# Kernel optimization log

Measured on AMD Instinct MI355X. Metric: run time of the kernel, lower is better.

Reference implementation:

```python
import jax, jax.numpy as jnp
import numpy as np
from jax import lax
from jax.scipy.special import logsumexp

B, T, Lc = 64, 512, 16
DW, CD, NF, KS, H, K, CV = 300, 50, 100, 3, 256, 9, 100
SCALE = 0.05


def setup_inputs() -> dict:
    key = jax.random.key(0)
    ks = jax.random.split(key, 20)
    f32 = jnp.float32
    return {
        'word_embs': jax.random.normal(ks[0], (B, T, DW), f32),
        'chars': jax.random.randint(ks[1], (B, T, Lc), 0, CV),
        'lengths': jax.random.randint(ks[2], (B,), T // 2, T + 1).astype(jnp.int32),
        'tags': jax.random.randint(ks[3], (B, T), 0, K),
        'fin_W': jax.random.normal(ks[4], (DW, DW), f32) * SCALE,
        'fin_b': jnp.zeros((DW,), f32),
        'char_emb': jax.random.normal(ks[5], (CV, CD), f32) * SCALE,
        'conv_W': jax.random.normal(ks[6], (KS, CD, NF), f32) * SCALE,  # (W, In, Out)
        'conv_b': jnp.zeros((NF,), f32),
        'Wih_f': jax.random.normal(ks[7], (4 * H, DW + NF), f32) * SCALE,
        'Whh_f': jax.random.normal(ks[8], (4 * H, H), f32) * SCALE,
        'b_f': jnp.zeros((4 * H,), f32),
        'Wih_b': jax.random.normal(ks[9], (4 * H, DW + NF), f32) * SCALE,
        'Whh_b': jax.random.normal(ks[10], (4 * H, H), f32) * SCALE,
        'b_b': jnp.zeros((4 * H,), f32),
        'out_W': jax.random.normal(ks[11], (2 * H, K), f32) * SCALE,
        'out_b': jnp.zeros((K,), f32),
        'trans': jax.random.normal(ks[12], (K, K), f32) * SCALE,
        'start_trans': jax.random.normal(ks[13], (K,), f32) * SCALE,
        'end_trans': jax.random.normal(ks[14], (K,), f32) * SCALE,
    }


def _lstm_scan(x, mask, Wih, Whh, b):
    # x: [B,T,D], mask: [B,T] bool -> outputs [B,T,H] (zeros at padding)
    xT = jnp.swapaxes(x, 0, 1)              # [T,B,D]
    mT = jnp.swapaxes(mask, 0, 1)           # [T,B]
    pre = jnp.einsum('tbd,gd->tbg', xT, Wih) + b  # precompute input part [T,B,4H]
    h0 = jnp.zeros((x.shape[0], Whh.shape[1]), x.dtype)

    def step(carry, inp):
        h, c = carry
        px, m = inp
        g = px + h @ Whh.T
        i, f, gg, o = jnp.split(g, 4, axis=-1)  # pytorch gate order i,f,g,o
        c_new = jax.nn.sigmoid(f) * c + jax.nn.sigmoid(i) * jnp.tanh(gg)
        h_new = jax.nn.sigmoid(o) * jnp.tanh(c_new)
        m = m[:, None]
        h2 = jnp.where(m, h_new, h)
        c2 = jnp.where(m, c_new, c)
        return (h2, c2), h2 * m

    _, hs = lax.scan(step, (h0, h0), (pre, mT))
    return jnp.swapaxes(hs, 0, 1)


def _reverse_by_length(x, lengths):
    # reverse the valid prefix of each sequence (padding stays at the end)
    t = jnp.arange(x.shape[1])
    rev = jnp.where(t[None, :] < lengths[:, None], lengths[:, None] - 1 - t[None, :], t[None, :])
    return jnp.take_along_axis(x, rev[:, :, None], axis=1)


def _crf_forward(logits, tags, mask, trans, start_trans, end_trans):
    # torchcrf-style log-likelihood; returns scalar sum over batch
    eT = jnp.swapaxes(logits, 0, 1)  # [T,B,K]
    mT = jnp.swapaxes(mask, 0, 1).astype(logits.dtype)  # [T,B]
    bidx = jnp.arange(logits.shape[0])
    # numerator: gold path score
    score = start_trans[tags[:, 0]] + eT[0][bidx, tags[:, 0]]

    def nstep(carry, inp):
        sc, prev = carry
        e, tg, m = inp
        step_sc = trans[prev, tg] + e[bidx, tg]
        sc = sc + m * step_sc
        prev = jnp.where(m > 0, tg, prev)
        return (sc, prev), None

    tT = jnp.swapaxes(tags, 0, 1)
    (score, last_tag), _ = lax.scan(nstep, (score, tags[:, 0]), (eT[1:], tT[1:], mT[1:]))
    score = score + end_trans[last_tag]
    # denominator: log-partition via forward algorithm
    alpha = start_trans[None, :] + eT[0]

    def fstep(a, inp):
        e, m = inp
        nxt = logsumexp(a[:, :, None] + trans[None, :, :] + e[:, None, :], axis=1)
        return jnp.where(m[:, None] > 0, nxt, a), None

    alpha, _ = lax.scan(fstep, alpha, (eT[1:], mT[1:]))
    Z = logsumexp(alpha + end_trans[None, :], axis=-1)
    return jnp.sum(score - Z)


def _viterbi(logits, mask, trans, start_trans, end_trans):
    eT = jnp.swapaxes(logits, 0, 1)  # [T,B,K]
    mT = jnp.swapaxes(mask, 0, 1)    # [T,B] bool
    Ktags = logits.shape[-1]
    ident = jnp.arange(Ktags)[None, :]

    def vstep(a, inp):
        e, m = inp
        cand = a[:, :, None] + trans[None, :, :]   # [B, K_prev, K_cur]
        bp = jnp.argmax(cand, axis=1)
        nxt = jnp.max(cand, axis=1) + e
        a2 = jnp.where(m[:, None], nxt, a)
        bp = jnp.where(m[:, None], bp, ident)       # identity backptr at padding
        return a2, bp

    alpha, bps = lax.scan(vstep, start_trans[None, :] + eT[0], (eT[1:], mT[1:]))
    last = jnp.argmax(alpha + end_trans[None, :], axis=-1)

    def bstep(tag, bp):
        prev = jnp.take_along_axis(bp, tag[:, None], axis=1)[:, 0]
        return prev, tag

    tag0, tail = lax.scan(bstep, last, bps, reverse=True)  # tail[t] = tag at time t+1
    path = jnp.concatenate([tag0[:, None], jnp.swapaxes(tail, 0, 1)], axis=1)  # [B,T]
    return path * mask  # zero-pad like zero_pad(preds)


def reference(word_embs, chars, lengths, tags, fin_W, fin_b, char_emb, conv_W, conv_b,
              Wih_f, Whh_f, b_f, Wih_b, Whh_b, b_b, out_W, out_b,
              trans, start_trans, end_trans):
    mask = jnp.arange(T)[None, :] < lengths[:, None]  # [B,T]
    # 1) word embeddings through finetune linear
    we = word_embs @ fin_W.T + fin_b
    # 2) char CNN: embed -> conv1d over chars -> relu -> max-pool
    ce = char_emb[chars].reshape(B * T, Lc, CD)
    conv = lax.conv_general_dilated(ce, conv_W, (1,), 'SAME',
                                    dimension_numbers=('NWC', 'WIO', 'NWC')) + conv_b
    char_feat = jnp.max(jax.nn.relu(conv), axis=1).reshape(B, T, NF)
    # 3) concat; 4) BiLSTM (dropout=0 / eval mode)
    x = jnp.concatenate([we, char_feat], axis=-1)
    h_fwd = _lstm_scan(x, mask, Wih_f, Whh_f, b_f)
    x_rev = _reverse_by_length(x, lengths)
    h_bwd = _reverse_by_length(_lstm_scan(x_rev, mask, Wih_b, Whh_b, b_b), lengths)
    lstm_out = jnp.concatenate([h_fwd, h_bwd], axis=-1)  # [B,T,2H]
    # 5) linear head; 6-7) CRF loss + viterbi decode
    logits = lstm_out @ out_W + out_b  # [B,T,K]
    loss = -_crf_forward(logits, tags, mask, trans, start_trans, end_trans)
    preds = _viterbi(logits, mask, trans, start_trans, end_trans)
    return loss, preds
```

## Files before the change

kernel.cpp:

```cpp
#include <hip/hip_runtime.h>


__device__ __forceinline__ float sigf(float x){ return 1.0f/(1.0f + expf(-x)); }

__global__ void pack_weights(const float* __restrict__ Wih_f, const float* __restrict__ Wih_b,
                             const float* __restrict__ Whh_f, const float* __restrict__ Whh_b,
                             const float* __restrict__ fin_W,
                             float4* __restrict__ Wp_f, float4* __restrict__ Wp_b,
                             float4* __restrict__ WT_f, float4* __restrict__ WT_b,
                             float* __restrict__ finWT){
  int stride = gridDim.x*blockDim.x;
  for (int idx = blockIdx.x*blockDim.x + threadIdx.x; idx < 425872; idx += stride){
    if (idx < 204800){
      int i2 = idx; const float* W = Wih_f; float4* P = Wp_f;
      if (i2 >= 102400){ i2 -= 102400; W = Wih_b; P = Wp_b; }
      int d = i2 >> 8, j = i2 & 255;
      P[i2] = make_float4(W[j*400+d], W[(j+256)*400+d], W[(j+512)*400+d], W[(j+768)*400+d]);
    } else if (idx < 335872){
      int i2 = idx - 204800; const float* W = Whh_f; float4* P = WT_f;
      if (i2 >= 65536){ i2 -= 65536; W = Whh_b; P = WT_b; }
      int d = i2 >> 8, j = i2 & 255;
      P[i2] = make_float4(W[j*256+d], W[(j+256)*256+d], W[(j+512)*256+d], W[(j+768)*256+d]);
    } else {
      int i2 = idx - 335872;
      int d = i2 / 300, j = i2 - d*300;
      finWT[d*304 + j] = fin_W[j*300 + d];
    }
  }
}

__global__ __launch_bounds__(256) void featurize(const float* __restrict__ we_in,
      const float* __restrict__ finWT, const float* __restrict__ finb,
      const int* __restrict__ chars, const float* __restrict__ char_emb,
      const float* __restrict__ convW, const float* __restrict__ convb,
      float* __restrict__ x){
  __shared__ __align__(16) char fsm[31104];
  int bid = blockIdx.x;
  int tid = threadIdx.x;
  if (bid < 2048){
    float* embT = (float*)fsm;
    int tok0 = bid * 16;
    for (int idx = tid; idx < 4800; idx += 256){
      int tt = idx / 300, d = idx - tt*300;
      embT[d*16 + tt] = we_in[(size_t)tok0*300 + idx];
    }
    __syncthreads();
    for (int j = tid; j < 300; j += 256){
      float bias = finb[j];
      float acc[16];
#pragma unroll
      for (int k2=0;k2<16;k2++) acc[k2]=bias;
      const float4* e4 = (const float4*)embT;
#pragma unroll 4
      for (int d=0; d<300; d++){
        float w = finWT[d*304 + j];
        float4 a = e4[d*4+0], b2 = e4[d*4+1], c2 = e4[d*4+2], d2 = e4[d*4+3];
        acc[0]+=a.x*w;  acc[1]+=a.y*w;  acc[2]+=a.z*w;  acc[3]+=a.w*w;
        acc[4]+=b2.x*w; acc[5]+=b2.y*w; acc[6]+=b2.z*w; acc[7]+=b2.w*w;
        acc[8]+=c2.x*w; acc[9]+=c2.y*w; acc[10]+=c2.z*w;acc[11]+=c2.w*w;
        acc[12]+=d2.x*w;acc[13]+=d2.y*w;acc[14]+=d2.z*w;acc[15]+=d2.w*w;
      }
#pragma unroll
      for (int k2=0;k2<16;k2++) x[(size_t)(tok0+k2)*400 + j] = acc[k2];
    }
  } else {
    float* ce2 = (float*)fsm;
    int* chs = (int*)(fsm + 30464);
    int tok0 = (bid - 2048) * 8;
    if (tid < 128) chs[tid] = chars[(size_t)tok0*16 + tid];
    __syncthreads();
    for (int idx = tid; idx < 7200; idx += 256){
      int tok = idx / 900; int r = idx - tok*900;
      int w1 = r / 50; int c = r - w1*50;
      float v = 0.f;
      if (w1 >= 1 && w1 <= 16) v = char_emb[chs[tok*16 + (w1-1)]*50 + c];
      ce2[tok*952 + c*19 + w1] = v;
    }
    __syncthreads();
    for (int p = tid; p < 800; p += 256){
      int tok = p / 100, f = p - tok*100;
      float s[16];
#pragma unroll
      for (int w=0; w<16; w++) s[w] = 0.f;
      const float* cebase = ce2 + tok*952;
      for (int c=0; c<50; c++){
        float cr[18];
#pragma unroll
        for (int i=0;i<18;i++) cr[i] = cebase[c*19+i];
#pragma unroll
        for (int k2=0;k2<3;k2++){
          float wv = convW[(k2*50+c)*100 + f];
#pragma unroll
          for (int w=0;w<16;w++) s[w] += cr[w+k2]*wv;
        }
      }
      float m = s[0];
#pragma unroll
      for (int w=1;w<16;w++) m = fmaxf(m, s[w]);
      m = fmaxf(0.f, m + convb[f]);
      x[(size_t)(tok0+tok)*400 + 300 + f] = m;
    }
  }
}

__global__ __launch_bounds__(256) void pre_gemm(const float* __restrict__ x,
     const float4* __restrict__ Wp_f, const float4* __restrict__ Wp_b,
     const float* __restrict__ b_f, const float* __restrict__ b_b,
     const int* __restrict__ lengths,
     float4* __restrict__ pre_f, float4* __restrict__ pre_b,
     int t0, int CH){
  int dir = blockIdx.z;
  const float4* Wp = dir ? Wp_b : Wp_f;
  const float* bias = dir ? b_b : b_f;
  float4* pre = dir ? pre_b : pre_f;
  int tok0 = blockIdx.x * 64;
  int j0 = blockIdx.y * 64;
  __shared__ float As[16][68];
  __shared__ float4 Bs[4][16][16];
  __shared__ int rows_s[64];
  __shared__ int poss_s[64];
  int tid = threadIdx.x;
  int tx = tid & 15, ty = tid >> 4;
  if (tid < 64){
    int tok = tok0 + tid;
    int b = tok / CH;
    int trel = tok - b*CH;
    int t = t0 + trel;
    int row;
    if (dir == 0) row = t;
    else { int len = lengths[b]; int pr = len - 1 - t; row = pr < 0 ? 0 : pr; }
    rows_s[tid] = b*512 + row;
    poss_s[tid] = b*128 + trel;
  }
  float4 acc[4][4];
#pragma unroll
  for (int s2=0;s2<4;s2++){
    int j = j0 + tx*4 + s2;
    float4 bj = make_float4(bias[j], bias[j+256], bias[j+512], bias[j+768]);
#pragma unroll
    for (int r=0;r<4;r++) acc[r][s2] = bj;
  }
  __syncthreads();
  int tokA = tid >> 2, kqA = tid & 3;
  int jjB = tid & 63,  kbB = tid >> 6;
  float4 aReg; float4 bReg[4];
  {
    aReg = *(const float4*)&x[(size_t)rows_s[tokA]*400 + 0 + kqA*4];
#pragma unroll
    for (int rr=0;rr<4;rr++) bReg[rr] = Wp[(size_t)(0 + kbB + rr*4)*256 + j0 + jjB];
  }
  for (int kt=0; kt<25; ++kt){
    As[kqA*4+0][tokA] = aReg.x;
    As[kqA*4+1][tokA] = aReg.y;
    As[kqA*4+2][tokA] = aReg.z;
    As[kqA*4+3][tokA] = aReg.w;
#pragma unroll
    for (int rr=0;rr<4;rr++) Bs[jjB&3][kbB+rr*4][jjB>>2] = bReg[rr];
    __syncthreads();
    if (kt < 24){
      int k0n = (kt+1)*16;
      aReg = *(const float4*)&x[(size_t)rows_s[tokA]*400 + k0n + kqA*4];
#pragma unroll
      for (int rr=0;rr<4;rr++) bReg[rr] = Wp[(size_t)(k0n + kbB + rr*4)*256 + j0 + jjB];
    }
#pragma unroll
    for (int kk=0; kk<16; ++kk){
      float4 a4 = *(const float4*)&As[kk][ty*4];
      float a[4] = {a4.x, a4.y, a4.z, a4.w};
#pragma unroll
      for (int s2=0;s2<4;s2++){
        float4 b4 = Bs[s2][kk][tx];
#pragma unroll
        for (int r=0;r<4;r++){
          acc[r][s2].x += a[r]*b4.x;
          acc[r][s2].y += a[r]*b4.y;
          acc[r][s2].z += a[r]*b4.z;
          acc[r][s2].w += a[r]*b4.w;
        }
      }
    }
    __syncthreads();
  }
#pragma unroll
  for (int r=0;r<4;r++){
    int pp = poss_s[ty*4+r];
#pragma unroll
    for (int s2=0;s2<4;s2++){
      pre[(size_t)pp*256 + j0 + tx*4 + s2] = acc[r][s2];
    }
  }
}

#define NRD 24
#define NLD 8
#define NSTREAM (64 - NRD - NLD)

#define OFF_WLDS 0
#define OFF_PART 131072
#define OFF_OWS  143360
#define OFF_H    152576
#define POOL_SZ  154624
#define PG_AS    0
#define PG_BS    4352
#define PG_ROWS  12544
#define PG_STRIDE 13056

__global__ __launch_bounds__(1024, 1)
void fused_scan_pre(const float4* __restrict__ prec_f, const float4* __restrict__ prec_b,
     float4* __restrict__ pren_f_w, float4* __restrict__ pren_b_w,
     const float4* __restrict__ WT_f, const float4* __restrict__ WT_b,
     const float4* __restrict__ Wp_f, const float4* __restrict__ Wp_b,
     const float* __restrict__ b_f, const float* __restrict__ b_b,
     const float* __restrict__ x, const int* __restrict__ lengths,
     const float* __restrict__ outW,
     float* __restrict__ logits_f, float* __restrict__ logits_b,
     float* __restrict__ st_h, float* __restrict__ st_c,
     int t0, int nsteps, int t0n, int cnext, int do_pre){
  __shared__ __align__(16) char smem[POOL_SZ];
  int wid = blockIdx.x;
  int tid = threadIdx.x;
  if (wid < 128){
    int dir = wid & 1;
    int b = wid >> 1;
    int len = lengths[b];
    if (len <= t0) return;
    const float4* pre = (dir ? prec_b : prec_f) + (size_t)b*128*256;
    const float4* WT = dir ? WT_b : WT_f;
    float* lg = (dir ? logits_b : logits_f) + (size_t)b*512*9;
    float4* wlds = (float4*)(smem + OFF_WLDS);
    float4* part = (float4*)(smem + OFF_PART);
    float*  oWs  = (float*)(smem + OFF_OWS);
    float*  hbuf = (float*)(smem + OFF_H);
    int j = tid & 255, q = tid >> 8;
    for (int i = tid; i < 2304; i += 1024) oWs[i] = outW[dir*2304 + i];
    for (int i = tid; i < 4*NLD*256; i += 1024){
      int qq = i >> 11;
      int rr = i & (NLD*256 - 1);
      int dl = rr >> 8, jj = rr & 255;
      wlds[(qq*NLD + dl)*256 + jj] = WT[(size_t)(qq*64 + NRD + dl)*256 + jj];
    }
    const float4* WTq = WT + (size_t)q*64*256;
    float4 wreg[NRD];
#pragma unroll
    for (int r=0; r<NRD; ++r) wreg[r] = WTq[(size_t)r*256 + j];
    float c = 0.f;
    if (t0 == 0){
      if (tid < 256) hbuf[tid] = 0.f;
    } else {
      if (tid < 256) hbuf[tid] = st_h[(dir*64+b)*256 + tid];
      if (q == 0) c = st_c[(dir*64+b)*256 + j];
    }
    __syncthreads();
    int tend = len < t0+nsteps ? len : t0+nsteps;
    const float4* WTs = WTq + (size_t)(NRD+NLD)*256 + j;
    int cur = 0;
    for (int t=t0; t<tend; ++t){
      const float* hc = hbuf + (cur << 8);
      const float* hq = hc + (q << 6);
      float4 p0;
      if (q == 0) p0 = pre[(size_t)(t - t0)*256 + j];
      float4 acc = make_float4(0.f,0.f,0.f,0.f);
#pragma unroll 8
      for (int s=0; s<NSTREAM; ++s){
        float hv = hq[NRD+NLD+s];
        float4 w = WTs[(size_t)s*256];
        acc.x += w.x*hv; acc.y += w.y*hv; acc.z += w.z*hv; acc.w += w.w*hv;
      }
#pragma unroll
      for (int r=0; r<NRD; ++r){
        float hv = hq[r];
        float4 w = wreg[r];
        acc.x += w.x*hv; acc.y += w.y*hv; acc.z += w.z*hv; acc.w += w.w*hv;
      }
#pragma unroll
      for (int l=0; l<NLD; ++l){
        float hv = hq[NRD+l];
        float4 w = wlds[(q*NLD + l)*256 + j];
        acc.x += w.x*hv; acc.y += w.y*hv; acc.z += w.z*hv; acc.w += w.w*hv;
      }
      if (q) part[((q-1)<<8) + j] = acc;
      if (t > t0 && tid < 576){
        int pprev = dir ? (len - t) : (t - 1);
        int k = tid >> 6, l = tid & 63;
        float s = hc[l]*oWs[l*9+k] + hc[l+64]*oWs[(l+64)*9+k]
                + hc[l+128]*oWs[(l+128)*9+k] + hc[l+192]*oWs[(l+192)*9+k];
#pragma unroll
        for (int o=32; o; o>>=1) s += __shfl_down(s, o, 64);
        if (l == 0) lg[pprev*9 + k] = s;
      }
      __syncthreads();
      if (q == 0){
        float4 p1 = part[j], p2 = part[256+j], p3 = part[512+j];
        float gi = acc.x + p0.x + p1.x + p2.x + p3.x;
        float gf = acc.y + p0.y + p1.y + p2.y + p3.y;
        float gg = acc.z + p0.z + p1.z + p2.z + p3.z;
        float go = acc.w + p0.w + p1.w + p2.w + p3.w;
        c = sigf(gf)*c + sigf(gi)*tanhf(gg);
        float h = sigf(go)*tanhf(c);
        hbuf[((cur^1)<<8) + j] = h;
      }
      __syncthreads();
      cur ^= 1;
    }
    const float* hc = hbuf + (cur << 8);
    if (tid < 576){
      int plast = dir ? (len - tend) : (tend - 1);
      int k = tid >> 6, l = tid & 63;
      float s = hc[l]*oWs[l*9+k] + hc[l+64]*oWs[(l+64)*9+k]
              + hc[l+128]*oWs[(l+128)*9+k] + hc[l+192]*oWs[(l+192)*9+k];
#pragma unroll
      for (int o=32; o; o>>=1) s += __shfl_down(s, o, 64);
      if (l == 0) lg[plast*9 + k] = s;
    }
    if (tid < 256) st_h[(dir*64+b)*256 + tid] = hc[tid];
    if (q == 0) st_c[(dir*64+b)*256 + j] = c;
  } else {
    if (!do_pre) return;
    int w = wid - 128;
    int g = tid >> 8, lt = tid & 255;
    char* gp = smem + g*PG_STRIDE;
    float (*As)[68] = (float(*)[68])(gp + PG_AS);
    float4* Bsl = (float4*)(gp + PG_BS);
    int* rows = (int*)(gp + PG_ROWS);
    int* poss = rows + 64;
    int tx = lt & 15, ty4 = (lt >> 4) * 4;
    int tokA = lt >> 2, kqA = lt & 3;
    int uB = lt & 31, kbB = lt >> 5;
    int tixmax = cnext << 4;
    int smax = (tixmax + 511) >> 9;
    for (int s=0; s<smax; ++s){
      int tix = s*512 + g*128 + w;
      bool active = tix < tixmax;
      int dir = tix & 1;
      int jh = (tix >> 1) & 7;
      int tokT = tix >> 4;
      int j0u = jh * 32;
      int tok0 = tokT * 64;
      const float4* Wp = dir ? Wp_b : Wp_f;
      const float* bias = dir ? b_b : b_f;
      float4* pren = dir ? pren_b_w : pren_f_w;
      __syncthreads();
      if (active && lt < 64){
        int tok = tok0 + lt;
        int bb = tok / cnext;
        int trel = tok - bb*cnext;
        int t = t0n + trel;
        int row;
        if (dir == 0) row = t;
        else { int len = lengths[bb]; int pr = len - 1 - t; row = pr < 0 ? 0 : pr; }
        rows[lt] = bb*512 + row;
        poss[lt] = bb*128 + trel;
      }
      float4 acc[4][2];
#pragma unroll
      for (int s2=0;s2<2;s2++){
        int u = j0u + tx + s2*16;
        float4 bj = make_float4(bias[u], bias[u+256], bias[u+512], bias[u+768]);
#pragma unroll
        for (int r=0;r<4;r++) acc[r][s2] = bj;
      }
      __syncthreads();
      for (int kt=0; kt<25; ++kt){
        int k0 = kt*16;
        if (active){
          const float* xr = x + (size_t)rows[tokA]*400 + k0 + kqA*4;
          float4 av = *(const float4*)xr;
          As[kqA*4+0][tokA]=av.x; As[kqA*4+1][tokA]=av.y;
          As[kqA*4+2][tokA]=av.z; As[kqA*4+3][tokA]=av.w;
          Bsl[kbB*32 + uB]     = Wp[(size_t)(k0+kbB)*256 + j0u + uB];
          Bsl[(kbB+8)*32 + uB] = Wp[(size_t)(k0+kbB+8)*256 + j0u + uB];
        }
        __syncthreads();
        if (active){
#pragma unroll 4
          for (int kk=0; kk<16; ++kk){
            float4 a4 = *(const float4*)&As[kk][ty4];
            float a0 = a4.x, a1 = a4.y, a2 = a4.z, a3 = a4.w;
            float4 b0 = Bsl[kk*32 + tx], b1 = Bsl[kk*32 + tx + 16];
            acc[0][0].x += a0*b0.x; acc[0][0].y += a0*b0.y; acc[0][0].z += a0*b0.z; acc[0][0].w += a0*b0.w;
            acc[1][0].x += a1*b0.x; acc[1][0].y += a1*b0.y; acc[1][0].z += a1*b0.z; acc[1][0].w += a1*b0.w;
            acc[2][0].x += a2*b0.x; acc[2][0].y += a2*b0.y; acc[2][0].z += a2*b0.z; acc[2][0].w += a2*b0.w;
            acc[3][0].x += a3*b0.x; acc[3][0].y += a3*b0.y; acc[3][0].z += a3*b0.z; acc[3][0].w += a3*b0.w;
            acc[0][1].x += a0*b1.x; acc[0][1].y += a0*b1.y; acc[0][1].z += a0*b1.z; acc[0][1].w += a0*b1.w;
            acc[1][1].x += a1*b1.x; acc[1][1].y += a1*b1.y; acc[1][1].z += a1*b1.z; acc[1][1].w += a1*b1.w;
            acc[2][1].x += a2*b1.x; acc[2][1].y += a2*b1.y; acc[2][1].z += a2*b1.z; acc[2][1].w += a2*b1.w;
            acc[3][1].x += a3*b1.x; acc[3][1].y += a3*b1.y; acc[3][1].z += a3*b1.z; acc[3][1].w += a3*b1.w;
          }
        }
        __syncthreads();
      }
      if (active){
#pragma unroll
        for (int r=0;r<4;r++){
          int pp = poss[ty4 + r];
          pren[(size_t)pp*256 + j0u + tx]      = acc[r][0];
          pren[(size_t)pp*256 + j0u + tx + 16] = acc[r][1];
        }
      }
    }
  }
}

__global__ __launch_bounds__(64) void crf_viterbi_kernel(const float* __restrict__ logits_f,
     const float* __restrict__ logits_b, const float* __restrict__ outb_,
     const int* __restrict__ tags, const int* __restrict__ lengths,
     const float* __restrict__ trans, const float* __restrict__ start_trans,
     const float* __restrict__ end_trans, float* __restrict__ loss_partial,
     float* __restrict__ preds){
  int wid = blockIdx.x;
  int is_crf = wid < 64 ? 1 : 0;
  int b = is_crf ? wid : wid - 64;
  int len = lengths[b];
  int tid = threadIdx.x;
  __shared__ float e_s[4608];
  __shared__ float tr[81];
  __shared__ float alpha[9];
  __shared__ int tg[512];
  __shared__ unsigned char bp[4608];
  const float* lf = logits_f + (size_t)b*4608;
  const float* lb = logits_b + (size_t)b*4608;
  for (int i=tid; i<4608; i+=64){
    int k = i - (i/9)*9;
    e_s[i] = lf[i] + lb[i] + outb_[k];
  }
  for (int i=tid; i<81; i+=64) tr[i] = trans[i];
  if (is_crf){
    for (int i=tid; i<512; i+=64) tg[i] = tags[b*512 + i];
    __syncthreads();
    if (tid < 9) alpha[tid] = start_trans[tid] + e_s[tid];
    __syncthreads();
    for (int t=1; t<len; ++t){
      float nxt = 0.f;
      if (tid < 9){
        float v[9];
#pragma unroll
        for (int j2=0;j2<9;j2++) v[j2] = alpha[j2] + tr[j2*9+tid];
        float m = v[0];
#pragma unroll
        for (int j2=1;j2<9;j2++) m = fmaxf(m, v[j2]);
        float ssum = 0.f;
#pragma unroll
        for (int j2=0;j2<9;j2++) ssum += expf(v[j2]-m);
        nxt = m + logf(ssum) + e_s[t*9+tid];
      }
      __syncthreads();
      if (tid < 9) alpha[tid] = nxt;
      __syncthreads();
    }
    if (tid == 0){
      float m = alpha[0] + end_trans[0];
      for (int k2=1;k2<9;k2++) m = fmaxf(m, alpha[k2]+end_trans[k2]);
      float ssum = 0.f;
      for (int k2=0;k2<9;k2++) ssum += expf(alpha[k2]+end_trans[k2]-m);
      float Z = m + logf(ssum);
      int prev = tg[0];
      float sc = start_trans[prev] + e_s[prev];
      for (int t=1;t<len;++t){
        int cur = tg[t];
        sc += tr[prev*9+cur] + e_s[t*9+cur];
        prev = cur;
      }
      sc += end_trans[prev];
      loss_partial[b] = Z - sc;
    }
  } else {
    __syncthreads();
    if (tid < 9) alpha[tid] = start_trans[tid] + e_s[tid];
    __syncthreads();
    for (int t=1; t<len; ++t){
      float nxt = 0.f; int bj = 0;
      if (tid < 9){
        float m = alpha[0] + tr[tid];
#pragma unroll
        for (int j2=1;j2<9;j2++){
          float v = alpha[j2] + tr[j2*9+tid];
          if (v > m){ m = v; bj = j2; }
        }
        nxt = m + e_s[t*9+tid];
      }
      __syncthreads();
      if (tid < 9){ alpha[tid] = nxt; bp[t*9+tid] = (unsigned char)bj; }
      __syncthreads();
    }
    for (int p2 = len + tid; p2 < 512; p2 += 64) preds[(size_t)b*512 + p2] = 0.f;
    if (tid == 0){
      float m = alpha[0] + end_trans[0]; int last = 0;
      for (int k2=1;k2<9;k2++){
        float v = alpha[k2] + end_trans[k2];
        if (v > m){ m = v; last = k2; }
      }
      int cur = last;
      preds[(size_t)b*512 + (len-1)] = (float)cur;
      for (int p2 = len-2; p2 >= 0; --p2){
        cur = bp[(p2+1)*9 + cur];
        preds[(size_t)b*512 + p2] = (float)cur;
      }
    }
  }
}

__global__ void loss_sum_kernel(const float* __restrict__ lp, float* __restrict__ out){
  float v = lp[threadIdx.x];
#pragma unroll
  for (int o=32; o; o>>=1) v += __shfl_down(v, o, 64);
  if (threadIdx.x == 0) out[0] = v;
}

extern "C" void kernel_launch(void* const* d_in, const int* in_sizes, int n_in,
                              void* d_out, int out_size, void* d_ws, size_t ws_size,
                              hipStream_t stream) {
  const float* word_embs  = (const float*)d_in[0];
  const int*   chars      = (const int*)  d_in[1];
  const int*   lengths    = (const int*)  d_in[2];
  const int*   tags       = (const int*)  d_in[3];
  const float* fin_W      = (const float*)d_in[4];
  const float* fin_b      = (const float*)d_in[5];
  const float* char_emb   = (const float*)d_in[6];
  const float* conv_W     = (const float*)d_in[7];
  const float* conv_b     = (const float*)d_in[8];
  const float* Wih_f      = (const float*)d_in[9];
  const float* Whh_f      = (const float*)d_in[10];
  const float* b_f        = (const float*)d_in[11];
  const float* Wih_b      = (const float*)d_in[12];
  const float* Whh_b      = (const float*)d_in[13];
  const float* b_b        = (const float*)d_in[14];
  const float* out_W      = (const float*)d_in[15];
  const float* out_b      = (const float*)d_in[16];
  const float* trans      = (const float*)d_in[17];
  const float* start_tr   = (const float*)d_in[18];
  const float* end_tr     = (const float*)d_in[19];

  float* ws = (float*)d_ws;
  float*  x         = ws;
  float4* Wp_f      = (float4*)(ws + 13107200);
  float4* Wp_b      = (float4*)(ws + 13516800);
  float4* WT_f      = (float4*)(ws + 13926400);
  float4* WT_b      = (float4*)(ws + 14188544);
  float*  finWT     = ws + 14450688;
  float*  logits_f  = ws + 14541888;
  float*  logits_b  = ws + 14836800;
  float*  st_h      = ws + 15131712;
  float*  st_c      = ws + 15164480;
  float*  loss_part = ws + 15197248;
  const size_t FIXED_F = 15197312;
  float4* preA_f = (float4*)(ws + FIXED_F);
  float4* preA_b = preA_f + (size_t)64*128*256;
  float4* preB_f = preA_b + (size_t)64*128*256;
  float4* preB_b = preB_f + (size_t)64*128*256;

  float* out = (float*)d_out;

  pack_weights<<<1664, 256, 0, stream>>>(Wih_f, Wih_b, Whh_f, Whh_b, fin_W,
                                         Wp_f, Wp_b, WT_f, WT_b, finWT);
  featurize<<<6144, 256, 0, stream>>>(word_embs, finWT, fin_b, chars, char_emb,
                                      conv_W, conv_b, x);

  pre_gemm<<<dim3(86, 4, 2), 256, 0, stream>>>(x, Wp_f, Wp_b, b_f, b_b, lengths,
                                               preA_f, preA_b, 0, 86);
  fused_scan_pre<<<256, 1024, 0, stream>>>(preA_f, preA_b, preB_f, preB_b,
      WT_f, WT_b, Wp_f, Wp_b, b_f, b_b, x, lengths, out_W,
      logits_f, logits_b, st_h, st_c, 0, 86, 86, 86, 1);
  fused_scan_pre<<<256, 1024, 0, stream>>>(preB_f, preB_b, preA_f, preA_b,
      WT_f, WT_b, Wp_f, Wp_b, b_f, b_b, x, lengths, out_W,
      logits_f, logits_b, st_h, st_c, 86, 86, 172, 85, 1);
  fused_scan_pre<<<256, 1024, 0, stream>>>(preA_f, preA_b, preB_f, preB_b,
      WT_f, WT_b, Wp_f, Wp_b, b_f, b_b, x, lengths, out_W,
      logits_f, logits_b, st_h, st_c, 172, 85, 257, 85, 1);
  fused_scan_pre<<<256, 1024, 0, stream>>>(preB_f, preB_b, preA_f, preA_b,
      WT_f, WT_b, Wp_f, Wp_b, b_f, b_b, x, lengths, out_W,
      logits_f, logits_b, st_h, st_c, 257, 85, 342, 85, 1);
  fused_scan_pre<<<256, 1024, 0, stream>>>(preA_f, preA_b, preB_f, preB_b,
      WT_f, WT_b, Wp_f, Wp_b, b_f, b_b, x, lengths, out_W,
      logits_f, logits_b, st_h, st_c, 342, 85, 427, 85, 1);
  fused_scan_pre<<<256, 1024, 0, stream>>>(preB_f, preB_b, preA_f, preA_b,
      WT_f, WT_b, Wp_f, Wp_b, b_f, b_b, x, lengths, out_W,
      logits_f, logits_b, st_h, st_c, 427, 85, 0, 85, 0);

  crf_viterbi_kernel<<<128, 64, 0, stream>>>(logits_f, logits_b, out_b, tags, lengths,
                                             trans, start_tr, end_tr, loss_part, out + 1);
  loss_sum_kernel<<<1, 64, 0, stream>>>(loss_part, out);
}
```

Baseline: 3.821 ms.

## Park recurrent weights in AGPRs and double-buffer the input-projection GEMM tiles

The recurrent scan now keeps 16 of the 64 per-thread Whh rows in accumulation registers (AGPRs) through inline asm. It cuts the VGPR-resident rows from 24 to 12, which leaves fewer rows streamed from global memory each step. The side-block input-projection GEMM gets double-buffered LDS tiles: the next k-tile is loaded into registers while the current one is computed, and each iteration needs one barrier instead of two. Costs are extra accvgpr read instructions on the serial recurrence path, more LDS per group, and a possible change in register allocation.

```diff
diff --git a/kernel.cpp b/kernel.cpp
--- a/kernel.cpp
+++ b/kernel.cpp
@@ -191,9 +191,23 @@
   }
 }
 
-#define NRD 24
+#define NRD 12
+#define NAG 16
 #define NLD 8
-#define NSTREAM (64 - NRD - NLD)
+#define NSTREAM (64 - NRD - NAG - NLD)
+
+#define AG_DECL(i) float agx##i, agy##i, agz##i, agw##i
+#define AG_WRITE(i, w) \
+  asm volatile("v_accvgpr_write_b32 %0, %1" : "=a"(agx##i) : "v"((w).x)); \
+  asm volatile("v_accvgpr_write_b32 %0, %1" : "=a"(agy##i) : "v"((w).y)); \
+  asm volatile("v_accvgpr_write_b32 %0, %1" : "=a"(agz##i) : "v"((w).z)); \
+  asm volatile("v_accvgpr_write_b32 %0, %1" : "=a"(agw##i) : "v"((w).w));
+#define AG_FMA(i, hv) { float tx_, ty_, tz_, tw_; \
+  asm volatile("v_accvgpr_read_b32 %0, %1" : "=v"(tx_) : "a"(agx##i)); \
+  asm volatile("v_accvgpr_read_b32 %0, %1" : "=v"(ty_) : "a"(agy##i)); \
+  asm volatile("v_accvgpr_read_b32 %0, %1" : "=v"(tz_) : "a"(agz##i)); \
+  asm volatile("v_accvgpr_read_b32 %0, %1" : "=v"(tw_) : "a"(agw##i)); \
+  acc.x += tx_*(hv); acc.y += ty_*(hv); acc.z += tz_*(hv); acc.w += tw_*(hv); }
 
 #define OFF_WLDS 0
 #define OFF_PART 131072
@@ -201,9 +215,9 @@
 #define OFF_H    152576
 #define POOL_SZ  154624
 #define PG_AS    0
-#define PG_BS    4352
-#define PG_ROWS  12544
-#define PG_STRIDE 13056
+#define PG_BS    8704
+#define PG_ROWS  25088
+#define PG_STRIDE 25600
 
 __global__ __launch_bounds__(1024, 1)
 void fused_scan_pre(const float4* __restrict__ prec_f, const float4* __restrict__ prec_b,
@@ -237,12 +251,35 @@
       int qq = i >> 11;
       int rr = i & (NLD*256 - 1);
       int dl = rr >> 8, jj = rr & 255;
-      wlds[(qq*NLD + dl)*256 + jj] = WT[(size_t)(qq*64 + NRD + dl)*256 + jj];
+      wlds[(qq*NLD + dl)*256 + jj] = WT[(size_t)(qq*64 + NRD + NAG + dl)*256 + jj];
     }
     const float4* WTq = WT + (size_t)q*64*256;
     float4 wreg[NRD];
 #pragma unroll
     for (int r=0; r<NRD; ++r) wreg[r] = WTq[(size_t)r*256 + j];
+    AG_DECL(0);  AG_DECL(1);  AG_DECL(2);  AG_DECL(3);
+    AG_DECL(4);  AG_DECL(5);  AG_DECL(6);  AG_DECL(7);
+    AG_DECL(8);  AG_DECL(9);  AG_DECL(10); AG_DECL(11);
+    AG_DECL(12); AG_DECL(13); AG_DECL(14); AG_DECL(15);
+    {
+      float4 w;
+      w = WTq[(size_t)(NRD+0)*256 + j];  AG_WRITE(0, w);
+      w = WTq[(size_t)(NRD+1)*256 + j];  AG_WRITE(1, w);
+      w = WTq[(size_t)(NRD+2)*256 + j];  AG_WRITE(2, w);
+      w = WTq[(size_t)(NRD+3)*256 + j];  AG_WRITE(3, w);
+      w = WTq[(size_t)(NRD+4)*256 + j];  AG_WRITE(4, w);
+      w = WTq[(size_t)(NRD+5)*256 + j];  AG_WRITE(5, w);
+      w = WTq[(size_t)(NRD+6)*256 + j];  AG_WRITE(6, w);
+      w = WTq[(size_t)(NRD+7)*256 + j];  AG_WRITE(7, w);
+      w = WTq[(size_t)(NRD+8)*256 + j];  AG_WRITE(8, w);
+      w = WTq[(size_t)(NRD+9)*256 + j];  AG_WRITE(9, w);
+      w = WTq[(size_t)(NRD+10)*256 + j]; AG_WRITE(10, w);
+      w = WTq[(size_t)(NRD+11)*256 + j]; AG_WRITE(11, w);
+      w = WTq[(size_t)(NRD+12)*256 + j]; AG_WRITE(12, w);
+      w = WTq[(size_t)(NRD+13)*256 + j]; AG_WRITE(13, w);
+      w = WTq[(size_t)(NRD+14)*256 + j]; AG_WRITE(14, w);
+      w = WTq[(size_t)(NRD+15)*256 + j]; AG_WRITE(15, w);
+    }
     float c = 0.f;
     if (t0 == 0){
       if (tid < 256) hbuf[tid] = 0.f;
@@ -252,7 +289,7 @@
     }
     __syncthreads();
     int tend = len < t0+nsteps ? len : t0+nsteps;
-    const float4* WTs = WTq + (size_t)(NRD+NLD)*256 + j;
+    const float4* WTs = WTq + (size_t)(NRD+NAG+NLD)*256 + j;
     int cur = 0;
     for (int t=t0; t<tend; ++t){
       const float* hc = hbuf + (cur << 8);
@@ -260,9 +297,9 @@
       float4 p0;
       if (q == 0) p0 = pre[(size_t)(t - t0)*256 + j];
       float4 acc = make_float4(0.f,0.f,0.f,0.f);
-#pragma unroll 8
+#pragma unroll 7
       for (int s=0; s<NSTREAM; ++s){
-        float hv = hq[NRD+NLD+s];
+        float hv = hq[NRD+NAG+NLD+s];
         float4 w = WTs[(size_t)s*256];
         acc.x += w.x*hv; acc.y += w.y*hv; acc.z += w.z*hv; acc.w += w.w*hv;
       }
@@ -272,9 +309,17 @@
         float4 w = wreg[r];
         acc.x += w.x*hv; acc.y += w.y*hv; acc.z += w.z*hv; acc.w += w.w*hv;
       }
+      AG_FMA(0,  hq[NRD+0]);  AG_FMA(1,  hq[NRD+1]);
+      AG_FMA(2,  hq[NRD+2]);  AG_FMA(3,  hq[NRD+3]);
+      AG_FMA(4,  hq[NRD+4]);  AG_FMA(5,  hq[NRD+5]);
+      AG_FMA(6,  hq[NRD+6]);  AG_FMA(7,  hq[NRD+7]);
+      AG_FMA(8,  hq[NRD+8]);  AG_FMA(9,  hq[NRD+9]);
+      AG_FMA(10, hq[NRD+10]); AG_FMA(11, hq[NRD+11]);
+      AG_FMA(12, hq[NRD+12]); AG_FMA(13, hq[NRD+13]);
+      AG_FMA(14, hq[NRD+14]); AG_FMA(15, hq[NRD+15]);
 #pragma unroll
       for (int l=0; l<NLD; ++l){
-        float hv = hq[NRD+l];
+        float hv = hq[NRD+NAG+l];
         float4 w = wlds[(q*NLD + l)*256 + j];
         acc.x += w.x*hv; acc.y += w.y*hv; acc.z += w.z*hv; acc.w += w.w*hv;
       }
@@ -319,8 +364,6 @@
     int w = wid - 128;
     int g = tid >> 8, lt = tid & 255;
     char* gp = smem + g*PG_STRIDE;
-    float (*As)[68] = (float(*)[68])(gp + PG_AS);
-    float4* Bsl = (float4*)(gp + PG_BS);
     int* rows = (int*)(gp + PG_ROWS);
     int* poss = rows + 64;
     int tx = lt & 15, ty4 = (lt >> 4) * 4;
@@ -360,23 +403,34 @@
         for (int r=0;r<4;r++) acc[r][s2] = bj;
       }
       __syncthreads();
+      if (active){
+        const float* xr = x + (size_t)rows[tokA]*400 + kqA*4;
+        float4 av = *(const float4*)xr;
+        float (*As0)[68] = (float(*)[68])(gp + PG_AS);
+        float4* Bs0 = (float4*)(gp + PG_BS);
+        As0[kqA*4+0][tokA]=av.x; As0[kqA*4+1][tokA]=av.y;
+        As0[kqA*4+2][tokA]=av.z; As0[kqA*4+3][tokA]=av.w;
+        Bs0[kbB*32 + uB]     = Wp[(size_t)(kbB)*256 + j0u + uB];
+        Bs0[(kbB+8)*32 + uB] = Wp[(size_t)(kbB+8)*256 + j0u + uB];
+      }
+      __syncthreads();
       for (int kt=0; kt<25; ++kt){
-        int k0 = kt*16;
-        if (active){
-          const float* xr = x + (size_t)rows[tokA]*400 + k0 + kqA*4;
-          float4 av = *(const float4*)xr;
-          As[kqA*4+0][tokA]=av.x; As[kqA*4+1][tokA]=av.y;
-          As[kqA*4+2][tokA]=av.z; As[kqA*4+3][tokA]=av.w;
-          Bsl[kbB*32 + uB]     = Wp[(size_t)(k0+kbB)*256 + j0u + uB];
-          Bsl[(kbB+8)*32 + uB] = Wp[(size_t)(k0+kbB+8)*256 + j0u + uB];
+        int bufc = kt & 1;
+        float (*Asc)[68] = (float(*)[68])(gp + PG_AS + bufc*4352);
+        float4* Bsc = (float4*)(gp + PG_BS + bufc*8192);
+        float4 av; float4 bv0, bv1;
+        if (active && kt < 24){
+          int k0n = (kt+1)*16;
+          av = *(const float4*)(x + (size_t)rows[tokA]*400 + k0n + kqA*4);
+          bv0 = Wp[(size_t)(k0n+kbB)*256 + j0u + uB];
+          bv1 = Wp[(size_t)(k0n+kbB+8)*256 + j0u + uB];
         }
-        __syncthreads();
         if (active){
 #pragma unroll 4
           for (int kk=0; kk<16; ++kk){
-            float4 a4 = *(const float4*)&As[kk][ty4];
+            float4 a4 = *(const float4*)&Asc[kk][ty4];
             float a0 = a4.x, a1 = a4.y, a2 = a4.z, a3 = a4.w;
-            float4 b0 = Bsl[kk*32 + tx], b1 = Bsl[kk*32 + tx + 16];
+            float4 b0 = Bsc[kk*32 + tx], b1 = Bsc[kk*32 + tx + 16];
             acc[0][0].x += a0*b0.x; acc[0][0].y += a0*b0.y; acc[0][0].z += a0*b0.z; acc[0][0].w += a0*b0.w;
             acc[1][0].x += a1*b0.x; acc[1][0].y += a1*b0.y; acc[1][0].z += a1*b0.z; acc[1][0].w += a1*b0.w;
             acc[2][0].x += a2*b0.x; acc[2][0].y += a2*b0.y; acc[2][0].z += a2*b0.z; acc[2][0].w += a2*b0.w;
@@ -385,6 +439,14 @@
             acc[1][1].x += a1*b1.x; acc[1][1].y += a1*b1.y; acc[1][1].z += a1*b1.z; acc[1][1].w += a1*b1.w;
             acc[2][1].x += a2*b1.x; acc[2][1].y += a2*b1.y; acc[2][1].z += a2*b1.z; acc[2][1].w += a2*b1.w;
             acc[3][1].x += a3*b1.x; acc[3][1].y += a3*b1.y; acc[3][1].z += a3*b1.z; acc[3][1].w += a3*b1.w;
+          }
+          if (kt < 24){
+            float (*Asn)[68] = (float(*)[68])(gp + PG_AS + (bufc^1)*4352);
+            float4* Bsn = (float4*)(gp + PG_BS + (bufc^1)*8192);
+            Asn[kqA*4+0][tokA]=av.x; Asn[kqA*4+1][tokA]=av.y;
+            Asn[kqA*4+2][tokA]=av.z; Asn[kqA*4+3][tokA]=av.w;
+            Bsn[kbB*32 + uB]     = bv0;
+            Bsn[(kbB+8)*32 + uB] = bv1;
           }
         }
         __syncthreads();
```

Result: slower. 4.627 ms (+21.1%).
